# Kernel optimization log

Measured on AMD Instinct MI355X. Metric: run time of the kernel, lower is better.

## Reference

```python
import jax, jax.numpy as jnp
import numpy as np

NUM_ITERATIONS = 3


def squash(t, axis=-1):
    # scale * t / ||t|| with scale = ||t||^2 / (1 + ||t||^2)
    sq = jnp.sum(t * t, axis=axis, keepdims=True)
    scale = sq / (1.0 + sq)
    return scale * t / jnp.sqrt(sq)


def setup_inputs() -> dict:
    key = jax.random.key(0)
    k1, k2 = jax.random.split(key)
    B, N, Ci = 256, 1152, 8   # batch, num_route_nodes, in_channels
    C, Co = 10, 16            # num_capsules, out_channels
    x = jax.random.normal(k1, (B, N, Ci), dtype=jnp.float32)
    route_weights = jax.random.normal(k2, (C, N, Ci, Co), dtype=jnp.float32)
    return {"x": x, "route_weights": route_weights}


def reference(x, route_weights):
    # priors: [C, B, N, 1, Co] (matches x[None,:,:,None,:] @ W[:,None])
    priors = jnp.einsum('bni,cnio->cbno', x, route_weights)[:, :, :, None, :]
    logits = jnp.zeros_like(priors)
    outputs = None
    for i in range(NUM_ITERATIONS):
        probs = jax.nn.softmax(logits, axis=2)  # softmax over route nodes (dim=2)
        outputs = squash(jnp.sum(probs * priors, axis=2, keepdims=True))  # [C,B,1,1,Co]
        if i != NUM_ITERATIONS - 1:
            # agreement: [C,B,N,1,1], broadcasts into logits
            logits = logits + jnp.sum(priors * outputs, axis=-1, keepdims=True)
    return outputs
```

## Files before the change

kernel.cpp:

```cpp
#include <hip/hip_runtime.h>
#include <hip/hip_fp16.h>

#define NB    384
#define ROWS  3
#define N_ROUTE 1152
#define C_IN  8
#define C_OUT 16
#define RS    9

template<int CTRL>
__device__ __forceinline__ float dpp_add(float v) {
    int t = __builtin_amdgcn_update_dpp(0, __float_as_int(v), CTRL, 0xF, 0xF, true);
    return v + __int_as_float(t);
}
__device__ __forceinline__ float wave_sum63(float v) {
    v = dpp_add<0x111>(v);
    v = dpp_add<0x112>(v);
    v = dpp_add<0x114>(v);
    v = dpp_add<0x118>(v);
    v = dpp_add<0x142>(v);
    v = dpp_add<0x143>(v);
    return v;
}

__global__ __launch_bounds__(NB, 2)
void capsule_routing(const float* __restrict__ x,
                     const float* __restrict__ W,
                     float* __restrict__ out)
{
    __shared__ unsigned int P[N_ROUTE * RS];
    __shared__ float red[6][20];
    __shared__ float vfin[16];

    const int t    = threadIdx.x;
    const int bid  = blockIdx.x;
    const int c    = bid >> 8;
    const int b    = bid & 255;
    const int lane = t & 63;
    const int wid  = t >> 6;

    {
        const int og = t & 3;
        const int nl = t >> 2;
        const float* __restrict__ xb = x + (size_t)b * (N_ROUTE * C_IN);
        const float* __restrict__ Wc = W + (size_t)c * (N_ROUTE * C_IN * C_OUT);
        #pragma unroll 2
        for (int pp = 0; pp < 12; ++pp) {
            const int n = pp * 96 + nl;
            const float4 x0 = *reinterpret_cast<const float4*>(xb + n * C_IN);
            const float4 x1 = *reinterpret_cast<const float4*>(xb + n * C_IN + 4);
            const float xs[8] = {x0.x, x0.y, x0.z, x0.w, x1.x, x1.y, x1.z, x1.w};
            const float* __restrict__ wp = Wc + (size_t)n * (C_IN * C_OUT) + (og << 2);
            float4 acc = make_float4(0.f, 0.f, 0.f, 0.f);
            #pragma unroll
            for (int i = 0; i < 8; ++i) {
                const float4 w = *reinterpret_cast<const float4*>(wp + i * C_OUT);
                acc.x = fmaf(xs[i], w.x, acc.x);
                acc.y = fmaf(xs[i], w.y, acc.y);
                acc.z = fmaf(xs[i], w.z, acc.z);
                acc.w = fmaf(xs[i], w.w, acc.w);
            }
            __half2 h0 = __floats2half2_rn(acc.x, acc.y);
            __half2 h1 = __floats2half2_rn(acc.z, acc.w);
            const int base = n * RS + (og << 1);
            P[base + 0] = *reinterpret_cast<unsigned int*>(&h0);
            P[base + 1] = *reinterpret_cast<unsigned int*>(&h1);
        }
    }
    __syncthreads();

    float vprev[16];
    #pragma unroll
    for (int o = 0; o < 16; ++o) vprev[o] = 0.f;
    float lg[ROWS] = {0.f, 0.f, 0.f};

    #pragma unroll
    for (int it = 0; it < 3; ++it) {
        float sp[16];
        #pragma unroll
        for (int o = 0; o < 16; ++o) sp[o] = 0.f;
        float zp = 0.f;

        #pragma unroll
        for (int k = 0; k < ROWS; ++k) {
            const int n = t + k * NB;
            const unsigned int* __restrict__ pr = &P[n * RS];
            float pv[16];
            #pragma unroll
            for (int j = 0; j < 8; ++j) {
                __half2 h = *reinterpret_cast<const __half2*>(&pr[j]);
                float2 f = __half22float2(h);
                pv[2 * j]     = f.x;
                pv[2 * j + 1] = f.y;
            }
            float d = 0.f;
            #pragma unroll
            for (int o = 0; o < 16; ++o) d = fmaf(pv[o], vprev[o], d);
            lg[k] += d;
            const float e = __expf(lg[k]);
            zp += e;
            #pragma unroll
            for (int o = 0; o < 16; ++o) sp[o] = fmaf(e, pv[o], sp[o]);
        }

        #pragma unroll
        for (int o = 0; o < 16; ++o) sp[o] = wave_sum63(sp[o]);
        zp = wave_sum63(zp);
        if (lane == 63) {
            #pragma unroll
            for (int o = 0; o < 16; ++o) red[wid][o] = sp[o];
            red[wid][16] = zp;
        }
        __syncthreads();

        if (t < 16) {
            float tot = 0.f, Zt = 0.f;
            #pragma unroll
            for (int w2 = 0; w2 < 6; ++w2) {
                tot += red[w2][t];
                Zt  += red[w2][16];
            }
            const float so = tot / Zt;
            float sq = so * so;
            #pragma unroll
            for (int off = 8; off >= 1; off >>= 1) sq += __shfl_xor(sq, off);
            const float fac = sqrtf(sq) / (1.f + sq);
            const float vo  = so * fac;
            if (it == 2) out[((size_t)bid << 4) + t] = vo;
            else         vfin[t] = vo;
        }
        if (it < 2) {
            __syncthreads();
            const float4 v0 = *reinterpret_cast<const float4*>(&vfin[0]);
            const float4 v1 = *reinterpret_cast<const float4*>(&vfin[4]);
            const float4 v2 = *reinterpret_cast<const float4*>(&vfin[8]);
            const float4 v3 = *reinterpret_cast<const float4*>(&vfin[12]);
            vprev[0]=v0.x;  vprev[1]=v0.y;  vprev[2]=v0.z;  vprev[3]=v0.w;
            vprev[4]=v1.x;  vprev[5]=v1.y;  vprev[6]=v1.z;  vprev[7]=v1.w;
            vprev[8]=v2.x;  vprev[9]=v2.y;  vprev[10]=v2.z; vprev[11]=v2.w;
            vprev[12]=v3.x; vprev[13]=v3.y; vprev[14]=v3.z; vprev[15]=v3.w;
        }
    }
}

extern "C" void kernel_launch(void* const* d_in, const int* in_sizes, int n_in,
                              void* d_out, int out_size, void* d_ws, size_t ws_size,
                              hipStream_t stream)
{
    const float* x   = (const float*)d_in[0];
    const float* W   = (const float*)d_in[1];
    float*       out = (float*)d_out;
    capsule_routing<<<dim3(10 * 256), dim3(NB), 0, stream>>>(x, W, out);
}
```

Baseline: 136.0 us.

## Process two batches per block with XCD-aware capsule mapping to reuse W loads

Each block now computes priors for two batch elements, so every loaded weight float4 feeds two FMA sets, halving W traffic per output. The block grows to 576 threads with 2 rows per thread, and the grid halves to 1280 blocks. Block IDs are remapped so each XCD mostly handles one capsule's weights, improving L2 locality. The cost is doubled shared memory per block (about 83 KB), which may limit occupancy, and the routing phases of the two batches run serially within the block.

```diff
diff --git a/kernel.cpp b/kernel.cpp
--- a/kernel.cpp
+++ b/kernel.cpp
@@ -1,12 +1,15 @@
 #include <hip/hip_runtime.h>
 #include <hip/hip_fp16.h>
 
-#define NB    384
-#define ROWS  3
+#define NB      576
+#define ROWS    2
+#define NBATCH  2
 #define N_ROUTE 1152
-#define C_IN  8
-#define C_OUT 16
-#define RS    9
+#define C_IN    8
+#define C_OUT   16
+#define RS      9
+#define NWAVE   9
+#define NPASS   8
 
 template<int CTRL>
 __device__ __forceinline__ float dpp_add(float v) {
@@ -23,122 +26,137 @@
     return v;
 }
 
-__global__ __launch_bounds__(NB, 2)
+__global__ __launch_bounds__(NB, 3)
 void capsule_routing(const float* __restrict__ x,
                      const float* __restrict__ W,
                      float* __restrict__ out)
 {
-    __shared__ unsigned int P[N_ROUTE * RS];
-    __shared__ float red[6][20];
+    __shared__ unsigned int P[NBATCH][N_ROUTE * RS];
+    __shared__ float red[NWAVE][20];
     __shared__ float vfin[16];
 
     const int t    = threadIdx.x;
-    const int bid  = blockIdx.x;
-    const int c    = bid >> 8;
-    const int b    = bid & 255;
     const int lane = t & 63;
     const int wid  = t >> 6;
+
+    const int g   = blockIdx.x;
+    const int xcd = g & 7;
+    const int j   = g >> 3;
+    int c, pb;
+    if (j < 128) { c = xcd;              pb = j; }
+    else         { const int jj = j - 128;
+                   c = 8 + (xcd >> 2);   pb = ((xcd & 3) << 5) + jj; }
+    const int b0 = pb << 1;
 
     {
         const int og = t & 3;
         const int nl = t >> 2;
-        const float* __restrict__ xb = x + (size_t)b * (N_ROUTE * C_IN);
-        const float* __restrict__ Wc = W + (size_t)c * (N_ROUTE * C_IN * C_OUT);
+        const float* __restrict__ xb0 = x + (size_t)b0 * (N_ROUTE * C_IN);
+        const float* __restrict__ xb1 = xb0 + (N_ROUTE * C_IN);
+        const float* __restrict__ Wc  = W + (size_t)c * (N_ROUTE * C_IN * C_OUT);
         #pragma unroll 2
-        for (int pp = 0; pp < 12; ++pp) {
-            const int n = pp * 96 + nl;
-            const float4 x0 = *reinterpret_cast<const float4*>(xb + n * C_IN);
-            const float4 x1 = *reinterpret_cast<const float4*>(xb + n * C_IN + 4);
-            const float xs[8] = {x0.x, x0.y, x0.z, x0.w, x1.x, x1.y, x1.z, x1.w};
+        for (int pp = 0; pp < NPASS; ++pp) {
+            const int n = pp * 144 + nl;
+            const float4 xa0 = *reinterpret_cast<const float4*>(xb0 + n * C_IN);
+            const float4 xa1 = *reinterpret_cast<const float4*>(xb0 + n * C_IN + 4);
+            const float4 xc0 = *reinterpret_cast<const float4*>(xb1 + n * C_IN);
+            const float4 xc1 = *reinterpret_cast<const float4*>(xb1 + n * C_IN + 4);
+            const float xs0[8] = {xa0.x, xa0.y, xa0.z, xa0.w, xa1.x, xa1.y, xa1.z, xa1.w};
+            const float xs1[8] = {xc0.x, xc0.y, xc0.z, xc0.w, xc1.x, xc1.y, xc1.z, xc1.w};
             const float* __restrict__ wp = Wc + (size_t)n * (C_IN * C_OUT) + (og << 2);
-            float4 acc = make_float4(0.f, 0.f, 0.f, 0.f);
+            float4 a0 = make_float4(0.f, 0.f, 0.f, 0.f);
+            float4 a1 = make_float4(0.f, 0.f, 0.f, 0.f);
             #pragma unroll
             for (int i = 0; i < 8; ++i) {
                 const float4 w = *reinterpret_cast<const float4*>(wp + i * C_OUT);
-                acc.x = fmaf(xs[i], w.x, acc.x);
-                acc.y = fmaf(xs[i], w.y, acc.y);
-                acc.z = fmaf(xs[i], w.z, acc.z);
-                acc.w = fmaf(xs[i], w.w, acc.w);
+                a0.x = fmaf(xs0[i], w.x, a0.x);  a1.x = fmaf(xs1[i], w.x, a1.x);
+                a0.y = fmaf(xs0[i], w.y, a0.y);  a1.y = fmaf(xs1[i], w.y, a1.y);
+                a0.z = fmaf(xs0[i], w.z, a0.z);  a1.z = fmaf(xs1[i], w.z, a1.z);
+                a0.w = fmaf(xs0[i], w.w, a0.w);  a1.w = fmaf(xs1[i], w.w, a1.w);
             }
-            __half2 h0 = __floats2half2_rn(acc.x, acc.y);
-            __half2 h1 = __floats2half2_rn(acc.z, acc.w);
             const int base = n * RS + (og << 1);
-            P[base + 0] = *reinterpret_cast<unsigned int*>(&h0);
-            P[base + 1] = *reinterpret_cast<unsigned int*>(&h1);
+            __half2 h;
+            h = __floats2half2_rn(a0.x, a0.y); P[0][base + 0] = *reinterpret_cast<unsigned int*>(&h);
+            h = __floats2half2_rn(a0.z, a0.w); P[0][base + 1] = *reinterpret_cast<unsigned int*>(&h);
+            h = __floats2half2_rn(a1.x, a1.y); P[1][base + 0] = *reinterpret_cast<unsigned int*>(&h);
+            h = __floats2half2_rn(a1.z, a1.w); P[1][base + 1] = *reinterpret_cast<unsigned int*>(&h);
         }
     }
     __syncthreads();
 
-    float vprev[16];
     #pragma unroll
-    for (int o = 0; o < 16; ++o) vprev[o] = 0.f;
-    float lg[ROWS] = {0.f, 0.f, 0.f};
-
-    #pragma unroll
-    for (int it = 0; it < 3; ++it) {
-        float sp[16];
+    for (int bt = 0; bt < NBATCH; ++bt) {
+        float vprev[16];
         #pragma unroll
-        for (int o = 0; o < 16; ++o) sp[o] = 0.f;
-        float zp = 0.f;
+        for (int o = 0; o < 16; ++o) vprev[o] = 0.f;
+        float lg[ROWS] = {0.f, 0.f};
 
         #pragma unroll
-        for (int k = 0; k < ROWS; ++k) {
-            const int n = t + k * NB;
-            const unsigned int* __restrict__ pr = &P[n * RS];
-            float pv[16];
+        for (int it = 0; it < 3; ++it) {
+            float sp[16];
             #pragma unroll
-            for (int j = 0; j < 8; ++j) {
-                __half2 h = *reinterpret_cast<const __half2*>(&pr[j]);
-                float2 f = __half22float2(h);
-                pv[2 * j]     = f.x;
-                pv[2 * j + 1] = f.y;
+            for (int o = 0; o < 16; ++o) sp[o] = 0.f;
+            float zp = 0.f;
+
+            #pragma unroll
+            for (int k = 0; k < ROWS; ++k) {
+                const unsigned int* __restrict__ pr = &P[bt][(t + k * NB) * RS];
+                float pv[16];
+                #pragma unroll
+                for (int jj = 0; jj < 8; ++jj) {
+                    __half2 h = *reinterpret_cast<const __half2*>(&pr[jj]);
+                    float2 f = __half22float2(h);
+                    pv[2 * jj]     = f.x;
+                    pv[2 * jj + 1] = f.y;
+                }
+                float d = 0.f;
+                #pragma unroll
+                for (int o = 0; o < 16; ++o) d = fmaf(pv[o], vprev[o], d);
+                lg[k] += d;
+                const float e = __expf(lg[k]);
+                zp += e;
+                #pragma unroll
+                for (int o = 0; o < 16; ++o) sp[o] = fmaf(e, pv[o], sp[o]);
             }
-            float d = 0.f;
+
             #pragma unroll
-            for (int o = 0; o < 16; ++o) d = fmaf(pv[o], vprev[o], d);
-            lg[k] += d;
-            const float e = __expf(lg[k]);
-            zp += e;
-            #pragma unroll
-            for (int o = 0; o < 16; ++o) sp[o] = fmaf(e, pv[o], sp[o]);
-        }
+            for (int o = 0; o < 16; ++o) sp[o] = wave_sum63(sp[o]);
+            zp = wave_sum63(zp);
+            if (lane == 63) {
+                #pragma unroll
+                for (int o = 0; o < 16; ++o) red[wid][o] = sp[o];
+                red[wid][16] = zp;
+            }
+            __syncthreads();
 
-        #pragma unroll
-        for (int o = 0; o < 16; ++o) sp[o] = wave_sum63(sp[o]);
-        zp = wave_sum63(zp);
-        if (lane == 63) {
-            #pragma unroll
-            for (int o = 0; o < 16; ++o) red[wid][o] = sp[o];
-            red[wid][16] = zp;
-        }
-        __syncthreads();
-
-        if (t < 16) {
-            float tot = 0.f, Zt = 0.f;
-            #pragma unroll
-            for (int w2 = 0; w2 < 6; ++w2) {
-                tot += red[w2][t];
-                Zt  += red[w2][16];
+            if (t < 16) {
+                float tot = 0.f, Zt = 0.f;
+                #pragma unroll
+                for (int w2 = 0; w2 < NWAVE; ++w2) {
+                    tot += red[w2][t];
+                    Zt  += red[w2][16];
+                }
+                const float so = tot / Zt;
+                float sq = so * so;
+                #pragma unroll
+                for (int off = 8; off >= 1; off >>= 1) sq += __shfl_xor(sq, off);
+                const float fac = sqrtf(sq) / (1.f + sq);
+                const float vo  = so * fac;
+                if (it == 2) out[((size_t)(((c << 8) + b0 + bt)) << 4) + t] = vo;
+                else         vfin[t] = vo;
             }
-            const float so = tot / Zt;
-            float sq = so * so;
-            #pragma unroll
-            for (int off = 8; off >= 1; off >>= 1) sq += __shfl_xor(sq, off);
-            const float fac = sqrtf(sq) / (1.f + sq);
-            const float vo  = so * fac;
-            if (it == 2) out[((size_t)bid << 4) + t] = vo;
-            else         vfin[t] = vo;
-        }
-        if (it < 2) {
-            __syncthreads();
-            const float4 v0 = *reinterpret_cast<const float4*>(&vfin[0]);
-            const float4 v1 = *reinterpret_cast<const float4*>(&vfin[4]);
-            const float4 v2 = *reinterpret_cast<const float4*>(&vfin[8]);
-            const float4 v3 = *reinterpret_cast<const float4*>(&vfin[12]);
-            vprev[0]=v0.x;  vprev[1]=v0.y;  vprev[2]=v0.z;  vprev[3]=v0.w;
-            vprev[4]=v1.x;  vprev[5]=v1.y;  vprev[6]=v1.z;  vprev[7]=v1.w;
-            vprev[8]=v2.x;  vprev[9]=v2.y;  vprev[10]=v2.z; vprev[11]=v2.w;
-            vprev[12]=v3.x; vprev[13]=v3.y; vprev[14]=v3.z; vprev[15]=v3.w;
+            if (!(bt == NBATCH - 1 && it == 2))
+                __syncthreads();
+            if (it < 2) {
+                const float4 v0 = *reinterpret_cast<const float4*>(&vfin[0]);
+                const float4 v1 = *reinterpret_cast<const float4*>(&vfin[4]);
+                const float4 v2 = *reinterpret_cast<const float4*>(&vfin[8]);
+                const float4 v3 = *reinterpret_cast<const float4*>(&vfin[12]);
+                vprev[0]=v0.x;  vprev[1]=v0.y;  vprev[2]=v0.z;  vprev[3]=v0.w;
+                vprev[4]=v1.x;  vprev[5]=v1.y;  vprev[6]=v1.z;  vprev[7]=v1.w;
+                vprev[8]=v2.x;  vprev[9]=v2.y;  vprev[10]=v2.z; vprev[11]=v2.w;
+                vprev[12]=v3.x; vprev[13]=v3.y; vprev[14]=v3.z; vprev[15]=v3.w;
+            }
         }
     }
 }
@@ -150,5 +168,5 @@
     const float* x   = (const float*)d_in[0];
     const float* W   = (const float*)d_in[1];
     float*       out = (float*)d_out;
-    capsule_routing<<<dim3(10 * 256), dim3(NB), 0, stream>>>(x, W, out);
+    capsule_routing<<<dim3(10 * 128), dim3(NB), 0, stream>>>(x, W, out);
 }
```

Result: slower. 159.3 us (+17.1%).

## Swizzle LDS prior layout with XOR and skip logit work in first iteration

Applied to the files above, without the earlier changes.

The prior tile in shared memory changes from a padded stride-9 layout to a dense stride-8 layout, with word positions XOR-swizzled by (n>>2)&7 so that bank conflicts stay low without padding. In the first routing iteration all logits are zero, so the dot product and exp are skipped (e=1) and the partition sum starts at ROWS. The aim is to cut LDS footprint and ALU work in the routing loop. The swizzle adds a little index arithmetic, and the non-vectorized per-word LDS reads may stay scalar.

```diff
diff --git a/kernel.cpp b/kernel.cpp
--- a/kernel.cpp
+++ b/kernel.cpp
@@ -6,7 +6,6 @@
 #define N_ROUTE 1152
 #define C_IN  8
 #define C_OUT 16
-#define RS    9
 
 template<int CTRL>
 __device__ __forceinline__ float dpp_add(float v) {
@@ -28,7 +27,7 @@
                      const float* __restrict__ W,
                      float* __restrict__ out)
 {
-    __shared__ unsigned int P[N_ROUTE * RS];
+    __shared__ unsigned int P[N_ROUTE * 8];
     __shared__ float red[6][20];
     __shared__ float vfin[16];
 
@@ -60,11 +59,12 @@
                 acc.z = fmaf(xs[i], w.z, acc.z);
                 acc.w = fmaf(xs[i], w.w, acc.w);
             }
+            const int s    = (n >> 2) & 7;
+            const int base = n << 3;
             __half2 h0 = __floats2half2_rn(acc.x, acc.y);
             __half2 h1 = __floats2half2_rn(acc.z, acc.w);
-            const int base = n * RS + (og << 1);
-            P[base + 0] = *reinterpret_cast<unsigned int*>(&h0);
-            P[base + 1] = *reinterpret_cast<unsigned int*>(&h1);
+            P[base + (((og << 1)    ) ^ s)] = *reinterpret_cast<unsigned int*>(&h0);
+            P[base + (((og << 1) + 1) ^ s)] = *reinterpret_cast<unsigned int*>(&h1);
         }
     }
     __syncthreads();
@@ -79,28 +79,38 @@
         float sp[16];
         #pragma unroll
         for (int o = 0; o < 16; ++o) sp[o] = 0.f;
-        float zp = 0.f;
+        float zp = (it == 0) ? (float)ROWS : 0.f;
 
         #pragma unroll
         for (int k = 0; k < ROWS; ++k) {
             const int n = t + k * NB;
-            const unsigned int* __restrict__ pr = &P[n * RS];
-            float pv[16];
+            const int s = (n >> 2) & 7;
+            const unsigned int* __restrict__ pr = &P[n << 3];
+            __half2 h[8];
             #pragma unroll
             for (int j = 0; j < 8; ++j) {
-                __half2 h = *reinterpret_cast<const __half2*>(&pr[j]);
-                float2 f = __half22float2(h);
-                pv[2 * j]     = f.x;
-                pv[2 * j + 1] = f.y;
+                const unsigned int w = pr[j ^ s];
+                h[j] = *reinterpret_cast<const __half2*>(&w);
             }
-            float d = 0.f;
+            float e;
+            if (it == 0) {
+                e = 1.f;
+            } else {
+                float d = 0.f;
+                #pragma unroll
+                for (int j = 0; j < 8; ++j) {
+                    d = fmaf(__low2float(h[j]),  vprev[2 * j],     d);
+                    d = fmaf(__high2float(h[j]), vprev[2 * j + 1], d);
+                }
+                lg[k] += d;
+                e = __expf(lg[k]);
+                zp += e;
+            }
             #pragma unroll
-            for (int o = 0; o < 16; ++o) d = fmaf(pv[o], vprev[o], d);
-            lg[k] += d;
-            const float e = __expf(lg[k]);
-            zp += e;
-            #pragma unroll
-            for (int o = 0; o < 16; ++o) sp[o] = fmaf(e, pv[o], sp[o]);
+            for (int j = 0; j < 8; ++j) {
+                sp[2 * j]     = fmaf(e, __low2float(h[j]),  sp[2 * j]);
+                sp[2 * j + 1] = fmaf(e, __high2float(h[j]), sp[2 * j + 1]);
+            }
         }
 
         #pragma unroll
```

Result: no change. 137.6 us (+1.1%).
